# Optimization experiments

Hardware: AMD Instinct MI355X
Metric: run time of the kernel (lower is better)

## Reference

```python
import math
import jax, jax.numpy as jnp
import numpy as np

B, S, HID = 1, 2048, 2880
H, HKV, D = 64, 8, 64
G = H // HKV  # num_key_value_groups = 8


def setup_inputs() -> dict:
    key = jax.random.key(0)
    ks = jax.random.split(key, 10)
    sd = 1.0 / math.sqrt(HID)
    hidden_states = jax.random.normal(ks[0], (B, S, HID), dtype=jnp.float32)
    # causal additive mask [B, 1, S, S]
    causal = jnp.tril(jnp.ones((S, S), dtype=bool))
    attention_mask = jnp.where(causal, 0.0, -1e9).astype(jnp.float32)[None, None]
    Wq = jax.random.normal(ks[1], (H * D, HID), dtype=jnp.float32) * sd
    bq = jax.random.normal(ks[2], (H * D,), dtype=jnp.float32) * 0.01
    Wk = jax.random.normal(ks[3], (HKV * D, HID), dtype=jnp.float32) * sd
    bk = jax.random.normal(ks[4], (HKV * D,), dtype=jnp.float32) * 0.01
    Wv = jax.random.normal(ks[5], (HKV * D, HID), dtype=jnp.float32) * sd
    bv = jax.random.normal(ks[6], (HKV * D,), dtype=jnp.float32) * 0.01
    Wo = jax.random.normal(ks[7], (HID, H * D), dtype=jnp.float32) * (1.0 / math.sqrt(H * D))
    bo = jax.random.normal(ks[8], (HID,), dtype=jnp.float32) * 0.01
    return {"hidden_states": hidden_states, "attention_mask": attention_mask,
            "Wq": Wq, "bq": bq, "Wk": Wk, "bk": bk, "Wv": Wv, "bv": bv,
            "Wo": Wo, "bo": bo}


def reference(hidden_states, attention_mask, Wq, bq, Wk, bk, Wv, bv, Wo, bo):
    b, s, _ = hidden_states.shape
    # projections
    q = hidden_states @ Wq.T + bq  # [b, s, H*D]
    k = hidden_states @ Wk.T + bk  # [b, s, HKV*D]
    v = hidden_states @ Wv.T + bv
    # torch q head index h maps to kv head h // G, so split H -> (HKV, G)
    q = q.reshape(b, s, HKV, G, D).transpose(0, 2, 3, 1, 4)   # [b, kv, g, s, d]
    k = k.reshape(b, s, HKV, D).transpose(0, 2, 1, 3)         # [b, kv, s, d]
    v = v.reshape(b, s, HKV, D).transpose(0, 2, 1, 3)
    # grouped-query attention without materializing repeated KV (same math as repeat_interleave)
    scores = jnp.einsum('bkgsd,bktd->bkgst', q, k) / math.sqrt(D)
    scores = scores + attention_mask[:, :, None]              # broadcast [b,1,1,s,t]
    attn = jax.nn.softmax(scores.astype(jnp.float32), axis=-1).astype(q.dtype)
    out = jnp.einsum('bkgst,bktd->bkgsd', attn, v)            # [b, kv, g, s, d]
    out = out.transpose(0, 3, 1, 2, 4).reshape(b, s, H * D)
    return out @ Wo.T + bo
```

## Files before the change

kernel.cpp:

```cpp
#include <hip/hip_runtime.h>
#include <hip/hip_bf16.h>
#include <cmath>

typedef __hip_bfloat16 bf16;
typedef __bf16 bf16x8 __attribute__((ext_vector_type(8)));
typedef float floatx4 __attribute__((ext_vector_type(4)));

__device__ inline floatx4 mfma16(bf16x8 a, bf16x8 b, floatx4 c) {
  return __builtin_amdgcn_mfma_f32_16x16x32_bf16(a, b, c, 0, 0, 0);
}

__device__ inline void async_ld16(const void* g, void* l) {
  __builtin_amdgcn_global_load_lds((const __attribute__((address_space(1))) void*)g,
                                   (__attribute__((address_space(3))) void*)l,
                                   16, 0, 0);
}

__device__ inline uint4 pack8(float4 a, float4 b) {
  union { uint4 u; bf16 h[8]; } t;
  t.h[0] = __float2bfloat16(a.x); t.h[1] = __float2bfloat16(a.y);
  t.h[2] = __float2bfloat16(a.z); t.h[3] = __float2bfloat16(a.w);
  t.h[4] = __float2bfloat16(b.x); t.h[5] = __float2bfloat16(b.y);
  t.h[6] = __float2bfloat16(b.z); t.h[7] = __float2bfloat16(b.w);
  return t.u;
}

__global__ __launch_bounds__(256)
void cvt_f32_bf16(const float* __restrict__ s, bf16* __restrict__ d, int n8) {
  const int i = blockIdx.x * 256 + threadIdx.x;
  if (i >= n8) return;
  const float4 a = ((const float4*)s)[2 * i];
  const float4 b = ((const float4*)s)[2 * i + 1];
  ((uint4*)d)[i] = pack8(a, b);
}

__global__ void concat_bias3(const float* __restrict__ q, const float* __restrict__ k,
                             const float* __restrict__ v, float* __restrict__ o) {
  const int i = blockIdx.x * 256 + threadIdx.x;
  if (i < 4096) o[i] = q[i];
  else if (i < 4608) o[i] = k[i - 4096];
  else o[i] = v[i - 4608];
}

#define QSCALE 0.1803368801111601f

template <int OUT_MODE>
__global__ __launch_bounds__(256)
void gemm_bt_db(const bf16* __restrict__ A, const bf16* __restrict__ B,
                const float* __restrict__ bias, void* __restrict__ Cp,
                void* __restrict__ Cqp, void* __restrict__ Ctp,
                int M, int N, int K, float qmul) {
  __shared__ __align__(16) bf16 sA[2][128 * 32];
  __shared__ __align__(16) bf16 sB[2][128 * 32];
  const int tid  = threadIdx.x;
  const int wave = tid >> 6;
  const int lane = tid & 63;
  const int quad = lane >> 4;
  const int l15  = lane & 15;

  const int nwg = gridDim.x * gridDim.y;
  const int lin = blockIdx.y * gridDim.x + blockIdx.x;
  const int L   = (lin & 7) * (nwg >> 3) + (lin >> 3);
  const int bm  = (L / gridDim.x) * 128;
  const int bn  = (L % gridDim.x) * 128;

  const int wm = (wave & 1) * 64;
  const int wn = (wave >> 1) * 64;

  floatx4 acc[4][4] = {};

  const int g0 = tid, g1 = tid + 256;
  const int arow0 = bm + (g0 >> 2), acol0 = (g0 & 3) * 8;
  const int arow1 = bm + (g1 >> 2), acol1 = (g1 & 3) * 8;
  int brow0 = bn + (g0 >> 2); if (brow0 >= N) brow0 = N - 1;
  int brow1 = bn + (g1 >> 2); if (brow1 >= N) brow1 = N - 1;

  const int nk = K >> 5;
  async_ld16(A + (size_t)arow0 * K + acol0, &sA[0][wave * 512]);
  async_ld16(A + (size_t)arow1 * K + acol1, &sA[0][2048 + wave * 512]);
  async_ld16(B + (size_t)brow0 * K + acol0, &sB[0][wave * 512]);
  async_ld16(B + (size_t)brow1 * K + acol1, &sB[0][2048 + wave * 512]);

  for (int kt = 0; kt < nk; ++kt) {
    __syncthreads();
    if (kt + 1 < nk) {
      const int k0 = (kt + 1) << 5;
      const int nb = (kt + 1) & 1;
      async_ld16(A + (size_t)arow0 * K + k0 + acol0, &sA[nb][wave * 512]);
      async_ld16(A + (size_t)arow1 * K + k0 + acol1, &sA[nb][2048 + wave * 512]);
      async_ld16(B + (size_t)brow0 * K + k0 + acol0, &sB[nb][wave * 512]);
      async_ld16(B + (size_t)brow1 * K + k0 + acol1, &sB[nb][2048 + wave * 512]);
    }
    const bf16* a = sA[kt & 1];
    const bf16* b = sB[kt & 1];

    bf16x8 aF[4], bF[4];
#pragma unroll
    for (int mi = 0; mi < 4; ++mi)
      aF[mi] = *(const bf16x8*)(a + (wm + mi * 16 + l15) * 32 + quad * 8);
#pragma unroll
    for (int ni = 0; ni < 4; ++ni)
      bF[ni] = *(const bf16x8*)(b + (wn + ni * 16 + l15) * 32 + quad * 8);
#pragma unroll
    for (int mi = 0; mi < 4; ++mi)
#pragma unroll
      for (int ni = 0; ni < 4; ++ni)
        acc[mi][ni] = mfma16(aF[mi], bF[ni], acc[mi][ni]);
  }

#pragma unroll
  for (int ni = 0; ni < 4; ++ni) {
    const int col = bn + wn + ni * 16 + l15;
    if (col >= N) continue;
    const float bv = bias[col];
#pragma unroll
    for (int mi = 0; mi < 4; ++mi) {
      const int row = bm + wm + mi * 16 + quad * 4;
#pragma unroll
      for (int r = 0; r < 4; ++r) {
        const float val = acc[mi][ni][r] + bv;
        if (OUT_MODE == 1) {
          ((float*)Cp)[(size_t)(row + r) * N + col] = val;
        } else {
          if (col < 4096)      ((bf16*)Cp)[(size_t)(row + r) * 4096 + col] = __float2bfloat16(val * qmul);
          else if (col < 4608) ((bf16*)Cqp)[(size_t)(row + r) * 512 + (col - 4096)] = __float2bfloat16(val);
          else                 ((bf16*)Ctp)[(size_t)(col - 4608) * M + row + r] = __float2bfloat16(val);
        }
      }
    }
  }
}

template <int A_BF, int B_BF, int OUT_MODE>
__global__ __launch_bounds__(256)
void gemm_bt_bias(const void* __restrict__ Ap, const void* __restrict__ Bp,
                  const float* __restrict__ bias, void* __restrict__ Cp,
                  void* __restrict__ Cqp, void* __restrict__ Ctp,
                  int M, int N, int K, float qmul) {
  __shared__ __align__(16) bf16 sA[128 * 32];
  __shared__ __align__(16) bf16 sB[128 * 32];
  const int tid  = threadIdx.x;
  const int wave = tid >> 6;
  const int lane = tid & 63;
  const int quad = lane >> 4;
  const int l15  = lane & 15;
  const int bm = blockIdx.y * 128;
  const int bn = blockIdx.x * 128;
  const int wm = (wave & 1) * 64;
  const int wn = (wave >> 1) * 64;

  floatx4 acc[4][4] = {};

  const int g0 = tid, g1 = tid + 256;
  const int arow0 = bm + (g0 >> 2), acol0 = (g0 & 3) * 8;
  const int arow1 = bm + (g1 >> 2), acol1 = (g1 & 3) * 8;
  int brow0 = bn + (g0 >> 2); if (brow0 >= N) brow0 = N - 1;
  int brow1 = bn + (g1 >> 2); if (brow1 >= N) brow1 = N - 1;

  for (int k0 = 0; k0 < K; k0 += 32) {
    __syncthreads();
    if (A_BF) {
      const bf16* A = (const bf16*)Ap;
      async_ld16(A + (size_t)arow0 * K + k0 + acol0, sA + wave * 512);
      async_ld16(A + (size_t)arow1 * K + k0 + acol1, sA + 2048 + wave * 512);
    } else {
      const float* A = (const float*)Ap;
      const float* p0 = A + (size_t)arow0 * K + k0 + acol0;
      const float* p1 = A + (size_t)arow1 * K + k0 + acol1;
      *(uint4*)(sA + tid * 8)        = pack8(*(const float4*)p0, *(const float4*)(p0 + 4));
      *(uint4*)(sA + 2048 + tid * 8) = pack8(*(const float4*)p1, *(const float4*)(p1 + 4));
    }
    if (B_BF) {
      const bf16* B = (const bf16*)Bp;
      async_ld16(B + (size_t)brow0 * K + k0 + acol0, sB + wave * 512);
      async_ld16(B + (size_t)brow1 * K + k0 + acol1, sB + 2048 + wave * 512);
    } else {
      const float* B = (const float*)Bp;
      const float* p0 = B + (size_t)brow0 * K + k0 + acol0;
      const float* p1 = B + (size_t)brow1 * K + k0 + acol1;
      *(uint4*)(sB + tid * 8)        = pack8(*(const float4*)p0, *(const float4*)(p0 + 4));
      *(uint4*)(sB + 2048 + tid * 8) = pack8(*(const float4*)p1, *(const float4*)(p1 + 4));
    }
    __syncthreads();

    bf16x8 aF[4], bF[4];
#pragma unroll
    for (int mi = 0; mi < 4; ++mi)
      aF[mi] = *(const bf16x8*)(sA + (wm + mi * 16 + l15) * 32 + quad * 8);
#pragma unroll
    for (int ni = 0; ni < 4; ++ni)
      bF[ni] = *(const bf16x8*)(sB + (wn + ni * 16 + l15) * 32 + quad * 8);
#pragma unroll
    for (int mi = 0; mi < 4; ++mi)
#pragma unroll
      for (int ni = 0; ni < 4; ++ni)
        acc[mi][ni] = mfma16(aF[mi], bF[ni], acc[mi][ni]);
  }

#pragma unroll
  for (int ni = 0; ni < 4; ++ni) {
    const int col = bn + wn + ni * 16 + l15;
    if (col >= N) continue;
    const float bv = bias[col];
#pragma unroll
    for (int mi = 0; mi < 4; ++mi) {
      const int row = bm + wm + mi * 16 + quad * 4;
#pragma unroll
      for (int r = 0; r < 4; ++r) {
        const float val = acc[mi][ni][r] + bv;
        if (OUT_MODE == 0) {
          ((bf16*)Cp)[(size_t)(row + r) * N + col] = __float2bfloat16(val * qmul);
        } else if (OUT_MODE == 1) {
          ((float*)Cp)[(size_t)(row + r) * N + col] = val;
        } else if (OUT_MODE == 2) {
          ((bf16*)Ctp)[(size_t)col * M + row + r] = __float2bfloat16(val);
        }
      }
    }
  }
}

__global__ __launch_bounds__(256)
void attn_fused(const bf16* __restrict__ Q, const bf16* __restrict__ Kc,
                const bf16* __restrict__ Vt, bf16* __restrict__ AO) {
  constexpr int HD = 4096, KD = 512, SEQ = 2048;
  constexpr float NEG = -1e30f;
  __shared__ __align__(16) bf16 sP[64 * 64];
  __shared__ __align__(16) bf16 sK[2][64 * 64];
  __shared__ __align__(16) bf16 sV[2][64 * 64];

  const int lin = blockIdx.y * 32 + blockIdx.x;
  const int L   = (lin & 7) * 256 + (lin >> 3);
  const int h   = L >> 5;
  const int qb  = 31 - (L & 31);
  const int kvh = h >> 3;
  const int tid = threadIdx.x, wave = tid >> 6, lane = tid & 63;
  const int quad = lane >> 4, l15 = lane & 15;
  const int sq0 = qb * 64;

  const int lrow = lane >> 3;
  const int lgr  = (lane & 7) ^ lrow;

  bf16x8 qf[2];
#pragma unroll
  for (int ks = 0; ks < 2; ++ks)
    qf[ks] = *(const bf16x8*)(Q + (size_t)(sq0 + wave * 16 + l15) * HD + h * 64 + ks * 32 + quad * 8);

  bf16x8 onesf;
#pragma unroll
  for (int i = 0; i < 8; ++i) onesf[i] = (__bf16)1.0f;

#pragma unroll
  for (int i = 0; i < 2; ++i) {
    const int c = wave * 2 + i;
    async_ld16(Kc + (size_t)(c * 8 + lrow) * KD + kvh * 64 + lgr * 8, &sK[0][c * 512]);
    async_ld16(Vt + (size_t)(kvh * 64 + c * 8 + lrow) * SEQ + lgr * 8, &sV[0][c * 512]);
  }

  floatx4 o_acc[4] = {};
  floatx4 o_sum = {};
  float m_run = NEG;

  for (int kt = 0; kt <= qb; ++kt) {
    const int st0 = kt * 64;
    __syncthreads();

    if (kt < qb) {
      const int st1 = st0 + 64;
      const int nb = (kt + 1) & 1;
#pragma unroll
      for (int i = 0; i < 2; ++i) {
        const int c = wave * 2 + i;
        async_ld16(Kc + (size_t)(st1 + c * 8 + lrow) * KD + kvh * 64 + lgr * 8, &sK[nb][c * 512]);
        async_ld16(Vt + (size_t)(kvh * 64 + c * 8 + lrow) * SEQ + st1 + lgr * 8, &sV[nb][c * 512]);
      }
    }
    const bf16* kb = sK[kt & 1];
    const bf16* vb = sV[kt & 1];

    floatx4 s_acc[4] = {};
#pragma unroll
    for (int ks = 0; ks < 2; ++ks) {
#pragma unroll
      for (int ni = 0; ni < 4; ++ni) {
        const bf16x8 kF = *(const bf16x8*)(kb + (ni * 16 + l15) * 64 + (((ks * 4 + quad) ^ (l15 & 7)) * 8));
        s_acc[ni] = mfma16(kF, qf[ks], s_acc[ni]);
      }
    }

    if (kt == qb) {
      const int qloc = wave * 16 + l15;
#pragma unroll
      for (int ni = 0; ni < 4; ++ni)
#pragma unroll
        for (int r = 0; r < 4; ++r)
          if (ni * 16 + quad * 4 + r > qloc) s_acc[ni][r] = NEG;
    }

    float t0 = fmaxf(fmaxf(s_acc[0][0], s_acc[0][1]), fmaxf(s_acc[0][2], s_acc[0][3]));
    float t1 = fmaxf(fmaxf(s_acc[1][0], s_acc[1][1]), fmaxf(s_acc[1][2], s_acc[1][3]));
    float t2 = fmaxf(fmaxf(s_acc[2][0], s_acc[2][1]), fmaxf(s_acc[2][2], s_acc[2][3]));
    float t3 = fmaxf(fmaxf(s_acc[3][0], s_acc[3][1]), fmaxf(s_acc[3][2], s_acc[3][3]));
    float tm = fmaxf(fmaxf(t0, t1), fmaxf(t2, t3));
    tm = fmaxf(tm, __shfl_xor(tm, 16));
    tm = fmaxf(tm, __shfl_xor(tm, 32));

    if (!__all(tm - m_run <= 8.0f)) {
      const float mn = fmaxf(m_run, tm);
      const float alpha = exp2f(m_run - mn);
      m_run = mn;
#pragma unroll
      for (int r = 0; r < 4; ++r) o_sum[r] *= alpha;
#pragma unroll
      for (int di = 0; di < 4; ++di)
#pragma unroll
        for (int r = 0; r < 4; ++r) o_acc[di][r] *= alpha;
    }

    const int prow = wave * 16 + l15;
#pragma unroll
    for (int ni = 0; ni < 4; ++ni) {
      union { uint2 u; bf16 hh[4]; } pk;
#pragma unroll
      for (int r = 0; r < 4; ++r)
        pk.hh[r] = __float2bfloat16(exp2f(s_acc[ni][r] - m_run));
      const int g = ni * 2 + (quad >> 1);
      *(uint2*)(sP + prow * 64 + ((g ^ (l15 & 7)) * 8) + (quad & 1) * 4) = pk.u;
    }

#pragma unroll
    for (int ks = 0; ks < 2; ++ks) {
      const bf16x8 pF = *(const bf16x8*)(sP + prow * 64 + (((ks * 4 + quad) ^ (l15 & 7)) * 8));
#pragma unroll
      for (int di = 0; di < 4; ++di) {
        const bf16x8 vF = *(const bf16x8*)(vb + (di * 16 + l15) * 64 + (((ks * 4 + quad) ^ (l15 & 7)) * 8));
        o_acc[di] = mfma16(vF, pF, o_acc[di]);
      }
      o_sum = mfma16(onesf, pF, o_sum);
    }
  }

  const float inv = 1.0f / o_sum[0];
  const int row = sq0 + wave * 16 + l15;
#pragma unroll
  for (int di = 0; di < 4; ++di) {
    union { uint2 u; bf16 hh[4]; } pk;
#pragma unroll
    for (int r = 0; r < 4; ++r)
      pk.hh[r] = __float2bfloat16(o_acc[di][r] * inv);
    *(uint2*)(AO + (size_t)row * HD + h * 64 + di * 16 + quad * 4) = pk.u;
  }
}

extern "C" void kernel_launch(void* const* d_in, const int* in_sizes, int n_in,
                              void* d_out, int out_size, void* d_ws, size_t ws_size,
                              hipStream_t stream) {
  const float* X  = (const float*)d_in[0];
  const float* Wq = (const float*)d_in[2];
  const float* bq = (const float*)d_in[3];
  const float* Wk = (const float*)d_in[4];
  const float* bk = (const float*)d_in[5];
  const float* Wv = (const float*)d_in[6];
  const float* bv = (const float*)d_in[7];
  const float* Wo = (const float*)d_in[8];
  const float* bo = (const float*)d_in[9];
  float* out = (float*)d_out;

  char* ws = (char*)d_ws;
  bf16* Qb = (bf16*)(ws);
  bf16* Kb = (bf16*)(ws + 16777216);
  bf16* Vt = (bf16*)(ws + 18874368);
  bf16* AO = (bf16*)(ws + 20971520);
  bf16*  Xb   = (bf16*)(ws + 37748736);
  bf16*  Wall = (bf16*)(ws + 49545216);
  bf16*  Wob  = (bf16*)(ws + 79036416);
  float* ball = (float*)(ws + 102629376);
  const size_t NEED = 102649856;

  dim3 blk(256);
  if (ws_size >= NEED) {
    cvt_f32_bf16<<<dim3(2048 * 2880 / 8 / 256), blk, 0, stream>>>(X, Xb, 2048 * 2880 / 8);
    cvt_f32_bf16<<<dim3(4096 * 2880 / 8 / 256), blk, 0, stream>>>(Wq, Wall, 4096 * 2880 / 8);
    cvt_f32_bf16<<<dim3(512 * 2880 / 8 / 256),  blk, 0, stream>>>(Wk, Wall + (size_t)4096 * 2880, 512 * 2880 / 8);
    cvt_f32_bf16<<<dim3(512 * 2880 / 8 / 256),  blk, 0, stream>>>(Wv, Wall + (size_t)4608 * 2880, 512 * 2880 / 8);
    cvt_f32_bf16<<<dim3(2880 * 4096 / 8 / 256), blk, 0, stream>>>(Wo, Wob, 2880 * 4096 / 8);
    concat_bias3<<<dim3(20), blk, 0, stream>>>(bq, bk, bv, ball);

    gemm_bt_db<4><<<dim3(40, 16), blk, 0, stream>>>(Xb, Wall, ball, Qb, Kb, Vt, 2048, 5120, 2880, QSCALE);
    attn_fused<<<dim3(32, 64), blk, 0, stream>>>(Qb, Kb, Vt, AO);
    gemm_bt_db<1><<<dim3(23, 16), blk, 0, stream>>>(AO, Wob, bo, out, nullptr, nullptr, 2048, 2880, 4096, 1.f);
  } else {
    gemm_bt_bias<0, 0, 0><<<dim3(32, 16), blk, 0, stream>>>(X, Wq, bq, Qb, nullptr, nullptr, 2048, 4096, 2880, QSCALE);
    gemm_bt_bias<0, 0, 0><<<dim3(4, 16),  blk, 0, stream>>>(X, Wk, bk, Kb, nullptr, nullptr, 2048, 512, 2880, 1.f);
    gemm_bt_bias<0, 0, 2><<<dim3(4, 16),  blk, 0, stream>>>(X, Wv, bv, nullptr, nullptr, Vt, 2048, 512, 2880, 1.f);
    attn_fused<<<dim3(32, 64), blk, 0, stream>>>(Qb, Kb, Vt, AO);
    gemm_bt_bias<1, 0, 1><<<dim3(23, 16), blk, 0, stream>>>(AO, Wo, bo, out, nullptr, nullptr, 2048, 2880, 4096, 1.f);
  }
}
```

Before: 447.9 us.

## Fuse fp32-to-bf16 weight conversion into GEMM B-tile loads

Drops the separate conversion kernels for Wq/Wk/Wv/Wo. The GEMM now reads fp32 weights directly into registers, packs them to bf16 and stores them into shared memory each k-step, picking the Q/K/V source by column block. This removes four launches plus the write and re-read of the bf16 weight copies. In exchange each GEMM tile re-reads fp32 weights (double the bytes) once per M-block, adds convert and store work to the main loop, and adds an extra barrier per k-iteration.

```diff
diff --git a/kernel.cpp b/kernel.cpp
--- a/kernel.cpp
+++ b/kernel.cpp
@@ -46,10 +46,11 @@
 
 template <int OUT_MODE>
 __global__ __launch_bounds__(256)
-void gemm_bt_db(const bf16* __restrict__ A, const bf16* __restrict__ B,
-                const float* __restrict__ bias, void* __restrict__ Cp,
-                void* __restrict__ Cqp, void* __restrict__ Ctp,
-                int M, int N, int K, float qmul) {
+void gemm_bf32(const bf16* __restrict__ A, const float* __restrict__ Bq,
+               const float* __restrict__ Bk, const float* __restrict__ Bv,
+               const float* __restrict__ bias, void* __restrict__ Cp,
+               void* __restrict__ Cqp, void* __restrict__ Ctp,
+               int M, int N, int K, float qmul) {
   __shared__ __align__(16) bf16 sA[2][128 * 32];
   __shared__ __align__(16) bf16 sB[2][128 * 32];
   const int tid  = threadIdx.x;
@@ -75,24 +76,40 @@
   int brow0 = bn + (g0 >> 2); if (brow0 >= N) brow0 = N - 1;
   int brow1 = bn + (g1 >> 2); if (brow1 >= N) brow1 = N - 1;
 
+  const float* B = Bq; int bro = 0;
+  if (OUT_MODE == 4) {
+    if (bn >= 4608)      { B = Bv; bro = 4608; }
+    else if (bn >= 4096) { B = Bk; bro = 4096; }
+  }
+  const float* bp0 = B + (size_t)(brow0 - bro) * K + acol0;
+  const float* bp1 = B + (size_t)(brow1 - bro) * K + acol1;
+
   const int nk = K >> 5;
   async_ld16(A + (size_t)arow0 * K + acol0, &sA[0][wave * 512]);
   async_ld16(A + (size_t)arow1 * K + acol1, &sA[0][2048 + wave * 512]);
-  async_ld16(B + (size_t)brow0 * K + acol0, &sB[0][wave * 512]);
-  async_ld16(B + (size_t)brow1 * K + acol1, &sB[0][2048 + wave * 512]);
+  float4 f00 = *(const float4*)(bp0);
+  float4 f01 = *(const float4*)(bp0 + 4);
+  float4 f10 = *(const float4*)(bp1);
+  float4 f11 = *(const float4*)(bp1 + 4);
 
   for (int kt = 0; kt < nk; ++kt) {
+    const int cur = kt & 1;
+    __syncthreads();
+    *(uint4*)(&sB[cur][tid * 8])        = pack8(f00, f01);
+    *(uint4*)(&sB[cur][2048 + tid * 8]) = pack8(f10, f11);
     __syncthreads();
     if (kt + 1 < nk) {
       const int k0 = (kt + 1) << 5;
       const int nb = (kt + 1) & 1;
       async_ld16(A + (size_t)arow0 * K + k0 + acol0, &sA[nb][wave * 512]);
       async_ld16(A + (size_t)arow1 * K + k0 + acol1, &sA[nb][2048 + wave * 512]);
-      async_ld16(B + (size_t)brow0 * K + k0 + acol0, &sB[nb][wave * 512]);
-      async_ld16(B + (size_t)brow1 * K + k0 + acol1, &sB[nb][2048 + wave * 512]);
-    }
-    const bf16* a = sA[kt & 1];
-    const bf16* b = sB[kt & 1];
+      f00 = *(const float4*)(bp0 + k0);
+      f01 = *(const float4*)(bp0 + k0 + 4);
+      f10 = *(const float4*)(bp1 + k0);
+      f11 = *(const float4*)(bp1 + k0 + 4);
+    }
+    const bf16* a = sA[cur];
+    const bf16* b = sB[cur];
 
     bf16x8 aF[4], bF[4];
 #pragma unroll
@@ -372,23 +389,17 @@
   bf16* Vt = (bf16*)(ws + 18874368);
   bf16* AO = (bf16*)(ws + 20971520);
   bf16*  Xb   = (bf16*)(ws + 37748736);
-  bf16*  Wall = (bf16*)(ws + 49545216);
-  bf16*  Wob  = (bf16*)(ws + 79036416);
-  float* ball = (float*)(ws + 102629376);
-  const size_t NEED = 102649856;
+  float* ball = (float*)(ws + 49545216);
+  const size_t NEED = 49565696;
 
   dim3 blk(256);
   if (ws_size >= NEED) {
     cvt_f32_bf16<<<dim3(2048 * 2880 / 8 / 256), blk, 0, stream>>>(X, Xb, 2048 * 2880 / 8);
-    cvt_f32_bf16<<<dim3(4096 * 2880 / 8 / 256), blk, 0, stream>>>(Wq, Wall, 4096 * 2880 / 8);
-    cvt_f32_bf16<<<dim3(512 * 2880 / 8 / 256),  blk, 0, stream>>>(Wk, Wall + (size_t)4096 * 2880, 512 * 2880 / 8);
-    cvt_f32_bf16<<<dim3(512 * 2880 / 8 / 256),  blk, 0, stream>>>(Wv, Wall + (size_t)4608 * 2880, 512 * 2880 / 8);
-    cvt_f32_bf16<<<dim3(2880 * 4096 / 8 / 256), blk, 0, stream>>>(Wo, Wob, 2880 * 4096 / 8);
     concat_bias3<<<dim3(20), blk, 0, stream>>>(bq, bk, bv, ball);
 
-    gemm_bt_db<4><<<dim3(40, 16), blk, 0, stream>>>(Xb, Wall, ball, Qb, Kb, Vt, 2048, 5120, 2880, QSCALE);
+    gemm_bf32<4><<<dim3(40, 16), blk, 0, stream>>>(Xb, Wq, Wk, Wv, ball, Qb, Kb, Vt, 2048, 5120, 2880, QSCALE);
     attn_fused<<<dim3(32, 64), blk, 0, stream>>>(Qb, Kb, Vt, AO);
-    gemm_bt_db<1><<<dim3(23, 16), blk, 0, stream>>>(AO, Wob, bo, out, nullptr, nullptr, 2048, 2880, 4096, 1.f);
+    gemm_bf32<1><<<dim3(23, 16), blk, 0, stream>>>(AO, Wo, nullptr, nullptr, bo, out, nullptr, nullptr, 2048, 2880, 4096, 1.f);
   } else {
     gemm_bt_bias<0, 0, 0><<<dim3(32, 16), blk, 0, stream>>>(X, Wq, bq, Qb, nullptr, nullptr, 2048, 4096, 2880, QSCALE);
     gemm_bt_bias<0, 0, 0><<<dim3(4, 16),  blk, 0, stream>>>(X, Wk, bk, Kb, nullptr, nullptr, 2048, 512, 2880, 1.f);
```

Result: slower. 521.7 us (+16.5%).
